# Kernel tuning notes

Measured on AMD Instinct MI355X. Metric: run time of the kernel, lower is better.

Reference implementation:

```python
import jax, jax.numpy as jnp
import numpy as np

TGT, BSZ, E = 256, 8, 256
SRC = 4096
H = 8
HD = E // H


def setup_inputs() -> dict:
    key = jax.random.key(0)
    ks = jax.random.split(key, 6)
    return {
        "query": jax.random.normal(ks[0], (TGT, BSZ, E), dtype=jnp.float32),
        "key": jax.random.normal(ks[1], (SRC, BSZ, E), dtype=jnp.float32),
        "value": jax.random.normal(ks[2], (SRC, BSZ, E), dtype=jnp.float32),
        "proposal_mask": jax.random.uniform(ks[3], (BSZ, TGT, SRC), dtype=jnp.float32),
        "out_proj_weight": jax.random.normal(ks[4], (E, E), dtype=jnp.float32) * (1.0 / np.sqrt(E)),
        "out_proj_bias": jax.random.normal(ks[5], (E,), dtype=jnp.float32) * 0.01,
    }


def reference(query, key, value, proposal_mask, out_proj_weight, out_proj_bias):
    tgt_len, bsz, embed_dim = query.shape
    src_len = key.shape[0]
    num_heads = H
    head_dim = embed_dim // num_heads

    # v: (src, bsz, E) -> (src, bsz*H, hd) -> (bsz*H, src, hd); index q = b*H + h
    v = value.reshape(src_len, bsz * num_heads, head_dim).transpose(1, 0, 2)

    # proposal_mask (bsz, tgt, src); torch loop+stack produces mask_nhead[b*H+h] = proposal_mask[b]
    mask_nhead = jnp.repeat(proposal_mask, num_heads, axis=0)  # (bsz*H, tgt, src)

    # weighted sum of values per head (no score compute)
    attn_output = jnp.einsum('qts,qsc->qtc', mask_nhead, v)  # (bsz*H, tgt, hd)

    # (bsz*H, tgt, hd) -> (tgt, bsz*H, hd) -> (tgt, bsz, E)
    attn_output = attn_output.transpose(1, 0, 2).reshape(tgt_len, bsz, embed_dim)

    # out projection (outDecoderLayer=False)
    attn_output = attn_output @ out_proj_weight.T + out_proj_bias

    # averaged weights: mask repeated per head -> mean over heads == proposal_mask
    attn_weights = mask_nhead.reshape(bsz, num_heads, tgt_len, src_len).sum(axis=1) / num_heads
    return attn_output, attn_weights
```

## Files before the change

kernel.cpp:

```cpp
#include <hip/hip_runtime.h>
#include <hip/hip_bf16.h>

#define TGT 256
#define BSZ 8
#define E   256
#define SRC 4096

typedef __attribute__((ext_vector_type(8))) short           bf16x8;
typedef __attribute__((ext_vector_type(4))) float           f32x4;
typedef __attribute__((ext_vector_type(4))) float           f4;
typedef __attribute__((ext_vector_type(8))) unsigned short  u16x8;
typedef __attribute__((ext_vector_type(4))) unsigned short  u16x4;

__device__ inline unsigned short f2b(float x) {
    union { __hip_bfloat16 h; unsigned short u; } cv;
    cv.h = __float2bfloat16(x);
    return cv.u;
}

__device__ inline bf16x8 cvt8v(const float* __restrict__ p) {
    f4 lo = *(const f4*)p;
    f4 hi = *(const f4*)(p + 4);
    bf16x8 r;
    #pragma unroll
    for (int j = 0; j < 4; ++j) {
        r[j]     = (short)f2b(lo[j]);
        r[4 + j] = (short)f2b(hi[j]);
    }
    return r;
}

__global__ __launch_bounds__(256) void transpose_v(
    const float* __restrict__ value, unsigned short* __restrict__ vt)
{
    __shared__ unsigned short tile[64 * 72];
    const int b  = blockIdx.z;
    const int e0 = blockIdx.y * 64;
    const int s0 = blockIdx.x * 64;
    const int tid = threadIdx.x;

    #pragma unroll
    for (int i = 0; i < 4; ++i) {
        int lin = i * 256 + tid;
        int sl  = (lin >> 2) & 63;
        int c4  = ((lin >> 8) << 2) | (lin & 3);
        f4 v = *(const f4*)(value + (size_t)(s0 + sl) * (BSZ * E)
                                  + (size_t)b * E + e0 + c4 * 4);
        #pragma unroll
        for (int j = 0; j < 4; ++j)
            tile[(c4 * 4 + j) * 72 + sl] = f2b(v[j]);
    }
    __syncthreads();
    #pragma unroll
    for (int i = 0; i < 2; ++i) {
        int lin = i * 256 + tid;
        int er  = lin >> 3;
        int c8  = lin & 7;
        u16x8 v = *(const u16x8*)(tile + er * 72 + c8 * 8);
        *(u16x8*)(vt + (size_t)b * E * SRC + (size_t)(e0 + er) * SRC + s0 + c8 * 8) = v;
    }
}

#define AP 136

__global__ __launch_bounds__(512) void gemm1_fused(
    const float* __restrict__ mask,
    const unsigned short* __restrict__ vt,
    float* __restrict__ out1,
    float* __restrict__ part)
{
    __shared__ unsigned short As[2][32 * AP];
    const int bx  = blockIdx.x;
    const int b   = bx & 7;
    const int tt  = (bx >> 3) & 7;
    const int kc  = bx >> 6;
    const int t0  = tt * 32;
    const int k0  = kc * 1024;
    const int tid = threadIdx.x;
    const int w    = tid >> 6;
    const int lane = tid & 63;
    const int quad = lane >> 4;
    const int l15  = lane & 15;

    const float* mbase = mask + (size_t)b * TGT * SRC + (size_t)t0 * SRC + k0;
    float*       obase = out1 + (size_t)b * TGT * SRC + (size_t)t0 * SRC + k0;
    const int sr0 = tid >> 5, sc0 = (tid & 31) * 4;
    const int sr1 = (512 + tid) >> 5, sc1 = sc0;

    const unsigned short* vrow0 = vt + (size_t)b * E * SRC
                                + (size_t)(w * 32 + l15) * SRC + k0;
    const unsigned short* vrow1 = vrow0 + 16 * SRC;

    f32x4 acc00 = {}, acc01 = {}, acc10 = {}, acc11 = {};

    {
        f4 v0 = *(const f4*)(mbase + (size_t)sr0 * SRC + sc0);
        f4 v1 = *(const f4*)(mbase + (size_t)(sr1 & 31) * SRC + sc1);
        *(f4*)(obase + (size_t)sr0 * SRC + sc0) = v0;
        *(f4*)(obase + (size_t)(sr1 & 31) * SRC + sc1) = v1;
        unsigned short* d0 = &As[0][sr0 * AP + sc0];
        unsigned short* d1 = &As[0][(sr1 & 31) * AP + sc1];
        #pragma unroll
        for (int j = 0; j < 4; ++j) { d0[j] = f2b(v0[j]); d1[j] = f2b(v1[j]); }
    }
    bf16x8 B0[4], B1[4];
    #pragma unroll
    for (int j = 0; j < 4; ++j) {
        B0[j] = *(const bf16x8*)(vrow0 + j * 32 + quad * 8);
        B1[j] = *(const bf16x8*)(vrow1 + j * 32 + quad * 8);
    }
    __syncthreads();

    for (int ks = 0; ks < 8; ++ks) {
        const int slab = ks & 1;
        bf16x8 nB0[4], nB1[4];
        if (ks < 7) {
            #pragma unroll
            for (int j = 0; j < 4; ++j) {
                nB0[j] = *(const bf16x8*)(vrow0 + (ks + 1) * 128 + j * 32 + quad * 8);
                nB1[j] = *(const bf16x8*)(vrow1 + (ks + 1) * 128 + j * 32 + quad * 8);
            }
        }
        f4 v0, v1;
        if (ks < 7) {
            v0 = *(const f4*)(mbase + (size_t)sr0 * SRC + (ks + 1) * 128 + sc0);
            v1 = *(const f4*)(mbase + (size_t)(sr1 & 31) * SRC + (ks + 1) * 128 + sc1);
        }

        #pragma unroll
        for (int j = 0; j < 4; ++j) {
            bf16x8 a0 = *(const bf16x8*)(&As[slab][(     l15) * AP + j * 32 + quad * 8]);
            bf16x8 a1 = *(const bf16x8*)(&As[slab][(16 + l15) * AP + j * 32 + quad * 8]);
            acc00 = __builtin_amdgcn_mfma_f32_16x16x32_bf16(a0, B0[j], acc00, 0, 0, 0);
            acc01 = __builtin_amdgcn_mfma_f32_16x16x32_bf16(a0, B1[j], acc01, 0, 0, 0);
            acc10 = __builtin_amdgcn_mfma_f32_16x16x32_bf16(a1, B0[j], acc10, 0, 0, 0);
            acc11 = __builtin_amdgcn_mfma_f32_16x16x32_bf16(a1, B1[j], acc11, 0, 0, 0);
        }

        if (ks < 7) {
            *(f4*)(obase + (size_t)sr0 * SRC + (ks + 1) * 128 + sc0) = v0;
            *(f4*)(obase + (size_t)(sr1 & 31) * SRC + (ks + 1) * 128 + sc1) = v1;
            unsigned short* d0 = &As[slab ^ 1][sr0 * AP + sc0];
            unsigned short* d1 = &As[slab ^ 1][(sr1 & 31) * AP + sc1];
            #pragma unroll
            for (int j = 0; j < 4; ++j) { d0[j] = f2b(v0[j]); d1[j] = f2b(v1[j]); }
            #pragma unroll
            for (int j = 0; j < 4; ++j) { B0[j] = nB0[j]; B1[j] = nB1[j]; }
        }
        __syncthreads();
    }

    float* pb = part + ((size_t)kc * BSZ + b) * TGT * E;
    #pragma unroll
    for (int r = 0; r < 4; ++r) {
        int rr0 = t0 + quad * 4 + r;
        int rr1 = rr0 + 16;
        int c0  = w * 32 + l15;
        pb[(size_t)rr0 * E + c0]      = acc00[r];
        pb[(size_t)rr0 * E + c0 + 16] = acc01[r];
        pb[(size_t)rr1 * E + c0]      = acc10[r];
        pb[(size_t)rr1 * E + c0 + 16] = acc11[r];
    }
}

#define PSTRIDE ((size_t)BSZ * TGT * E)

__global__ __launch_bounds__(256) void gemm2(
    const float* __restrict__ part,
    const float* __restrict__ wgt,
    const float* __restrict__ bias,
    float* __restrict__ out0)
{
    const int tid  = threadIdx.x;
    const int wv   = tid >> 6;
    const int lane = tid & 63;
    const int tau  = blockIdx.x * 4 + wv;
    const int b    = tau >> 8;
    const int rem  = tau & 255;
    const int t0   = (rem >> 4) * 16;
    const int e0   = (rem & 15) * 16;
    const int quad = lane >> 4;
    const int l15  = lane & 15;

    const float* arow = part + (size_t)b * TGT * E + (size_t)(t0 + l15) * E + quad * 8;
    const float* brow = wgt + (size_t)(e0 + l15) * E + quad * 8;

    f32x4 acc = {};
    #pragma unroll
    for (int ks = 0; ks < 8; ++ks) {
        const float* ap = arow + ks * 32;
        f4 lo = *(const f4*)(ap);
        f4 hi = *(const f4*)(ap + 4);
        #pragma unroll
        for (int p = 1; p < 4; ++p) {
            lo += *(const f4*)(ap + p * PSTRIDE);
            hi += *(const f4*)(ap + p * PSTRIDE + 4);
        }
        bf16x8 a;
        #pragma unroll
        for (int j = 0; j < 4; ++j) {
            a[j]     = (short)f2b(lo[j]);
            a[4 + j] = (short)f2b(hi[j]);
        }
        bf16x8 bb = cvt8v(brow + ks * 32);
        acc = __builtin_amdgcn_mfma_f32_16x16x32_bf16(a, bb, acc, 0, 0, 0);
    }

    const float bval = bias[e0 + l15];
    #pragma unroll
    for (int r = 0; r < 4; ++r) {
        int t = t0 + quad * 4 + r;
        int e = e0 + l15;
        out0[(size_t)t * (BSZ * E) + (size_t)b * E + e] = acc[r] + bval;
    }
}

extern "C" void kernel_launch(void* const* d_in, const int* in_sizes, int n_in,
                              void* d_out, int out_size, void* d_ws, size_t ws_size,
                              hipStream_t stream)
{
    const float* value = (const float*)d_in[2];
    const float* mask  = (const float*)d_in[3];
    const float* wgt   = (const float*)d_in[4];
    const float* bias  = (const float*)d_in[5];

    float* out0 = (float*)d_out;
    float* out1 = (float*)d_out + (size_t)TGT * BSZ * E;

    unsigned short* vt   = (unsigned short*)d_ws;
    float*          part = (float*)(vt + (size_t)BSZ * E * SRC);

    transpose_v<<<dim3(SRC / 64, E / 64, BSZ), 256, 0, stream>>>(value, vt);
    gemm1_fused<<<256, 512, 0, stream>>>(mask, vt, out1, part);
    gemm2<<<512, 256, 0, stream>>>(part, wgt, bias, out0);
}
```

Measured before the change: 170.0 us.

## Fuse value transpose and bf16 conversion into gemm1 via shared-memory staging

Removes the separate transpose_v kernel and its bf16 workspace round-trip. gemm1 now reads fp32 value directly, converts it to bf16 and stores it transposed into a double-buffered shared tile. The K loop is restructured into 32 steps of 32, with a barrier each step. In exchange, each of the 8 t-tiles re-reads value from global memory, and per-lane strided scalar loads plus extra barriers may lower efficiency.

```diff
diff --git a/kernel.cpp b/kernel.cpp
--- a/kernel.cpp
+++ b/kernel.cpp
@@ -9,7 +9,6 @@
 typedef __attribute__((ext_vector_type(8))) short           bf16x8;
 typedef __attribute__((ext_vector_type(4))) float           f32x4;
 typedef __attribute__((ext_vector_type(4))) float           f4;
-typedef __attribute__((ext_vector_type(8))) unsigned short  u16x8;
 typedef __attribute__((ext_vector_type(4))) unsigned short  u16x4;
 
 __device__ inline unsigned short f2b(float x) {
@@ -30,46 +29,18 @@
     return r;
 }
 
-__global__ __launch_bounds__(256) void transpose_v(
-    const float* __restrict__ value, unsigned short* __restrict__ vt)
-{
-    __shared__ unsigned short tile[64 * 72];
-    const int b  = blockIdx.z;
-    const int e0 = blockIdx.y * 64;
-    const int s0 = blockIdx.x * 64;
-    const int tid = threadIdx.x;
-
-    #pragma unroll
-    for (int i = 0; i < 4; ++i) {
-        int lin = i * 256 + tid;
-        int sl  = (lin >> 2) & 63;
-        int c4  = ((lin >> 8) << 2) | (lin & 3);
-        f4 v = *(const f4*)(value + (size_t)(s0 + sl) * (BSZ * E)
-                                  + (size_t)b * E + e0 + c4 * 4);
-        #pragma unroll
-        for (int j = 0; j < 4; ++j)
-            tile[(c4 * 4 + j) * 72 + sl] = f2b(v[j]);
-    }
-    __syncthreads();
-    #pragma unroll
-    for (int i = 0; i < 2; ++i) {
-        int lin = i * 256 + tid;
-        int er  = lin >> 3;
-        int c8  = lin & 7;
-        u16x8 v = *(const u16x8*)(tile + er * 72 + c8 * 8);
-        *(u16x8*)(vt + (size_t)b * E * SRC + (size_t)(e0 + er) * SRC + s0 + c8 * 8) = v;
-    }
-}
-
 #define AP 136
+#define VP 40
 
 __global__ __launch_bounds__(512) void gemm1_fused(
+    const float* __restrict__ value,
     const float* __restrict__ mask,
-    const unsigned short* __restrict__ vt,
     float* __restrict__ out1,
     float* __restrict__ part)
 {
     __shared__ unsigned short As[2][32 * AP];
+    __shared__ unsigned short Vs[2][256 * VP];
+
     const int bx  = blockIdx.x;
     const int b   = bx & 7;
     const int tt  = (bx >> 3) & 7;
@@ -82,70 +53,90 @@
     const int quad = lane >> 4;
     const int l15  = lane & 15;
 
+    const int sr0 = tid >> 5;
+    const int sr1 = sr0 + 16;
+    const int sc  = (tid & 31) * 4;
     const float* mbase = mask + (size_t)b * TGT * SRC + (size_t)t0 * SRC + k0;
     float*       obase = out1 + (size_t)b * TGT * SRC + (size_t)t0 * SRC + k0;
-    const int sr0 = tid >> 5, sc0 = (tid & 31) * 4;
-    const int sr1 = (512 + tid) >> 5, sc1 = sc0;
-
-    const unsigned short* vrow0 = vt + (size_t)b * E * SRC
-                                + (size_t)(w * 32 + l15) * SRC + k0;
-    const unsigned short* vrow1 = vrow0 + 16 * SRC;
+
+    const int ve  = tid & 255;
+    const int vkg = (tid >> 8) * 16;
+    const float* vbase = value + (size_t)k0 * (BSZ * E) + (size_t)b * E + ve;
 
     f32x4 acc00 = {}, acc01 = {}, acc10 = {}, acc11 = {};
 
     {
-        f4 v0 = *(const f4*)(mbase + (size_t)sr0 * SRC + sc0);
-        f4 v1 = *(const f4*)(mbase + (size_t)(sr1 & 31) * SRC + sc1);
-        *(f4*)(obase + (size_t)sr0 * SRC + sc0) = v0;
-        *(f4*)(obase + (size_t)(sr1 & 31) * SRC + sc1) = v1;
-        unsigned short* d0 = &As[0][sr0 * AP + sc0];
-        unsigned short* d1 = &As[0][(sr1 & 31) * AP + sc1];
+        f4 v0 = *(const f4*)(mbase + (size_t)sr0 * SRC + sc);
+        f4 v1 = *(const f4*)(mbase + (size_t)sr1 * SRC + sc);
+        *(f4*)(obase + (size_t)sr0 * SRC + sc) = v0;
+        *(f4*)(obase + (size_t)sr1 * SRC + sc) = v1;
+        unsigned short* d0 = &As[0][sr0 * AP + sc];
+        unsigned short* d1 = &As[0][sr1 * AP + sc];
         #pragma unroll
         for (int j = 0; j < 4; ++j) { d0[j] = f2b(v0[j]); d1[j] = f2b(v1[j]); }
-    }
-    bf16x8 B0[4], B1[4];
-    #pragma unroll
-    for (int j = 0; j < 4; ++j) {
-        B0[j] = *(const bf16x8*)(vrow0 + j * 32 + quad * 8);
-        B1[j] = *(const bf16x8*)(vrow1 + j * 32 + quad * 8);
+
+        const float* vp = vbase + (size_t)vkg * (BSZ * E);
+        float vv[16];
+        #pragma unroll
+        for (int i = 0; i < 16; ++i) vv[i] = vp[(size_t)i * (BSZ * E)];
+        #pragma unroll
+        for (int g = 0; g < 4; ++g) {
+            u16x4 pk;
+            #pragma unroll
+            for (int c = 0; c < 4; ++c) pk[c] = f2b(vv[g * 4 + c]);
+            *(u16x4*)&Vs[0][ve * VP + vkg + g * 4] = pk;
+        }
     }
     __syncthreads();
 
-    for (int ks = 0; ks < 8; ++ks) {
-        const int slab = ks & 1;
-        bf16x8 nB0[4], nB1[4];
-        if (ks < 7) {
-            #pragma unroll
-            for (int j = 0; j < 4; ++j) {
-                nB0[j] = *(const bf16x8*)(vrow0 + (ks + 1) * 128 + j * 32 + quad * 8);
-                nB1[j] = *(const bf16x8*)(vrow1 + (ks + 1) * 128 + j * 32 + quad * 8);
+    for (int s = 0; s < 32; ++s) {
+        const int vb = s & 1;
+        const int ab = (s >> 2) & 1;
+        const int haveV = (s < 31);
+        const int haveA = ((s & 3) == 0) && (s < 28);
+
+        float vv[16];
+        if (haveV) {
+            const float* vp = vbase + (size_t)((s + 1) * 32 + vkg) * (BSZ * E);
+            #pragma unroll
+            for (int i = 0; i < 16; ++i) vv[i] = vp[(size_t)i * (BSZ * E)];
+        }
+        f4 a0v, a1v;
+        if (haveA) {
+            int ka = ((s >> 2) + 1) * 128;
+            a0v = *(const f4*)(mbase + (size_t)sr0 * SRC + ka + sc);
+            a1v = *(const f4*)(mbase + (size_t)sr1 * SRC + ka + sc);
+        }
+
+        {
+            const int koff = (s & 3) * 32 + quad * 8;
+            bf16x8 a0 = *(const bf16x8*)&As[ab][ l15       * AP + koff];
+            bf16x8 a1 = *(const bf16x8*)&As[ab][(l15 + 16) * AP + koff];
+            bf16x8 b0 = *(const bf16x8*)&Vs[vb][(w * 32 + l15)      * VP + quad * 8];
+            bf16x8 b1 = *(const bf16x8*)&Vs[vb][(w * 32 + l15 + 16) * VP + quad * 8];
+            acc00 = __builtin_amdgcn_mfma_f32_16x16x32_bf16(a0, b0, acc00, 0, 0, 0);
+            acc01 = __builtin_amdgcn_mfma_f32_16x16x32_bf16(a0, b1, acc01, 0, 0, 0);
+            acc10 = __builtin_amdgcn_mfma_f32_16x16x32_bf16(a1, b0, acc10, 0, 0, 0);
+            acc11 = __builtin_amdgcn_mfma_f32_16x16x32_bf16(a1, b1, acc11, 0, 0, 0);
+        }
+
+        if (haveA) {
+            int ka = ((s >> 2) + 1) * 128;
+            *(f4*)(obase + (size_t)sr0 * SRC + ka + sc) = a0v;
+            *(f4*)(obase + (size_t)sr1 * SRC + ka + sc) = a1v;
+            unsigned short* d0 = &As[ab ^ 1][sr0 * AP + sc];
+            unsigned short* d1 = &As[ab ^ 1][sr1 * AP + sc];
+            #pragma unroll
+            for (int j = 0; j < 4; ++j) { d0[j] = f2b(a0v[j]); d1[j] = f2b(a1v[j]); }
+        }
+        if (haveV) {
+            #pragma unroll
+            for (int g = 0; g < 4; ++g) {
+                u16x4 pk;
+                #pragma unroll
+                for (int c = 0; c < 4; ++c) pk[c] = f2b(vv[g * 4 + c]);
+                *(u16x4*)&Vs[vb ^ 1][ve * VP + vkg + g * 4] = pk;
             }
-        }
-        f4 v0, v1;
-        if (ks < 7) {
-            v0 = *(const f4*)(mbase + (size_t)sr0 * SRC + (ks + 1) * 128 + sc0);
-            v1 = *(const f4*)(mbase + (size_t)(sr1 & 31) * SRC + (ks + 1) * 128 + sc1);
-        }
-
-        #pragma unroll
-        for (int j = 0; j < 4; ++j) {
-            bf16x8 a0 = *(const bf16x8*)(&As[slab][(     l15) * AP + j * 32 + quad * 8]);
-            bf16x8 a1 = *(const bf16x8*)(&As[slab][(16 + l15) * AP + j * 32 + quad * 8]);
-            acc00 = __builtin_amdgcn_mfma_f32_16x16x32_bf16(a0, B0[j], acc00, 0, 0, 0);
-            acc01 = __builtin_amdgcn_mfma_f32_16x16x32_bf16(a0, B1[j], acc01, 0, 0, 0);
-            acc10 = __builtin_amdgcn_mfma_f32_16x16x32_bf16(a1, B0[j], acc10, 0, 0, 0);
-            acc11 = __builtin_amdgcn_mfma_f32_16x16x32_bf16(a1, B1[j], acc11, 0, 0, 0);
-        }
-
-        if (ks < 7) {
-            *(f4*)(obase + (size_t)sr0 * SRC + (ks + 1) * 128 + sc0) = v0;
-            *(f4*)(obase + (size_t)(sr1 & 31) * SRC + (ks + 1) * 128 + sc1) = v1;
-            unsigned short* d0 = &As[slab ^ 1][sr0 * AP + sc0];
-            unsigned short* d1 = &As[slab ^ 1][(sr1 & 31) * AP + sc1];
-            #pragma unroll
-            for (int j = 0; j < 4; ++j) { d0[j] = f2b(v0[j]); d1[j] = f2b(v1[j]); }
-            #pragma unroll
-            for (int j = 0; j < 4; ++j) { B0[j] = nB0[j]; B1[j] = nB1[j]; }
         }
         __syncthreads();
     }
@@ -227,10 +218,8 @@
     float* out0 = (float*)d_out;
     float* out1 = (float*)d_out + (size_t)TGT * BSZ * E;
 
-    unsigned short* vt   = (unsigned short*)d_ws;
-    float*          part = (float*)(vt + (size_t)BSZ * E * SRC);
-
-    transpose_v<<<dim3(SRC / 64, E / 64, BSZ), 256, 0, stream>>>(value, vt);
-    gemm1_fused<<<256, 512, 0, stream>>>(mask, vt, out1, part);
+    float* part = (float*)d_ws;
+
+    gemm1_fused<<<256, 512, 0, stream>>>(value, mask, out1, part);
     gemm2<<<512, 256, 0, stream>>>(part, wgt, bias, out0);
 }
```

Result: slower. 178.3 us (+4.8%).
